# Kernel tuning notes

Measured on AMD Instinct MI355X. Metric: run time of the kernel, lower is better.

The kernel has to match this reference:

```python
import jax, jax.numpy as jnp
import numpy as np
from jax import lax


def setup_inputs() -> dict:
    key = jax.random.key(0)
    k1, k2, k3 = jax.random.split(key, 3)
    X = jax.random.normal(k1, (8192, 8192), dtype=jnp.float32)
    K = jax.random.normal(k2, (7, 7), dtype=jnp.float32)
    bias = jax.random.normal(k3, (1,), dtype=jnp.float32)
    return {"X": X, "K": K, "bias": bias}


def reference(X, K, bias):
    # Valid 2D cross-correlation of X [H, W] with K [kh, kw], plus scalar bias.
    # Output shape: [H - kh + 1, W - kw + 1].
    lhs = X[None, None, :, :]          # NCHW, N=C=1
    rhs = K[None, None, :, :]          # OIHW, O=I=1
    out = lax.conv_general_dilated(
        lhs, rhs,
        window_strides=(1, 1),
        padding='VALID',
        dimension_numbers=('NCHW', 'OIHW', 'NCHW'),
    )
    return out[0, 0] + bias[0]
```

## Files before the change

### kernel.cpp

```cpp
#include <hip/hip_runtime.h>
#include <hip/hip_bf16.h>

#define IN_N    8192
#define OUT_N   8186
#define KS      7

#define SCOLS   512
#define OCOLS   496
#define NSTRIP  17
#define NSEG    60
#define NBLK    (NSTRIP * NSEG)
#define NROWB   38
#define LSTR    1040
#define NT8     31
#define TOTSTEP 512

typedef __bf16 bf16x8 __attribute__((ext_vector_type(8)));
typedef float  f32x4  __attribute__((ext_vector_type(4)));

union BFU { __bf16 h; unsigned short u; };
__device__ __forceinline__ unsigned short f2bf(float f) {
    BFU c; c.h = (__bf16)f; return c.u;
}

template<bool G>
__device__ __forceinline__ void run_strip(
    const float* __restrict__ X, float* __restrict__ out,
    char* sb, const bf16x8* bfrag, float bv,
    int X0, int s0, int s1, int tid)
{
    const int lane = tid & 63;
    const int wv   = tid >> 6;
    const int lo   = lane & 15;
    const int hi   = lane >> 4;
    const int p    = tid >> 7;
    const int cg   = tid & 127;
    const int ccol = X0 + 4 * cg;
    const int wcol = cg * 8;

    int wbase = (16 * s0 + 22 + p) % NROWB;

    int roff[KS];
    #pragma unroll
    for (int ky = 0; ky < KS; ++ky)
        roff[ky] = ((16 * s0 + lo + ky) % NROWB) * LSTR + 16 * hi;

    #pragma unroll
    for (int k = 0; k < 11; ++k) {
        int r = 16 * s0 + 2 * k + p;
        int c = ccol;
        if (G) { r = min(r, IN_N - 1); c = min(c, IN_N - 4); }
        float4 v = *(const float4*)(X + (size_t)r * IN_N + c);
        ushort4 h;
        h.x = f2bf(v.x); h.y = f2bf(v.y); h.z = f2bf(v.z); h.w = f2bf(v.w);
        const int slot = (16 * s0 + 2 * k + p) % NROWB;
        *(ushort4*)(sb + slot * LSTR + wcol) = h;
    }
    asm volatile("s_waitcnt lgkmcnt(0)" ::: "memory");
    __builtin_amdgcn_s_barrier();
    __builtin_amdgcn_sched_barrier(0);

    float4 ld[8];
    for (int s = s0; s < s1; ++s) {
        const int Y = 16 * s;
        const bool pre = (s + 1 < s1);

        if (pre) {
            #pragma unroll
            for (int k = 0; k < 8; ++k) {
                int r = Y + 22 + 2 * k + p;
                int c = ccol;
                if (G) { r = min(r, IN_N - 1); c = min(c, IN_N - 4); }
                ld[k] = *(const float4*)(X + (size_t)r * IN_N + c);
            }
        }
        __builtin_amdgcn_sched_barrier(0);

        for (int t8 = wv; t8 < NT8; t8 += 4) {
            const int off = 32 * t8;
            f32x4 accA = { bv, bv, bv, bv };
            f32x4 accB = { 0.f, 0.f, 0.f, 0.f };
            bf16x8 a0 = *(const bf16x8*)(sb + roff[0] + off);
            bf16x8 a1 = *(const bf16x8*)(sb + roff[1] + off);
            bf16x8 a2 = *(const bf16x8*)(sb + roff[2] + off);
            bf16x8 a3 = *(const bf16x8*)(sb + roff[3] + off);
            bf16x8 a4 = *(const bf16x8*)(sb + roff[4] + off);
            bf16x8 a5 = *(const bf16x8*)(sb + roff[5] + off);
            bf16x8 a6 = *(const bf16x8*)(sb + roff[6] + off);
            accA = __builtin_amdgcn_mfma_f32_16x16x32_bf16(bfrag[0], a0, accA, 0, 0, 0);
            accB = __builtin_amdgcn_mfma_f32_16x16x32_bf16(bfrag[1], a1, accB, 0, 0, 0);
            accA = __builtin_amdgcn_mfma_f32_16x16x32_bf16(bfrag[2], a2, accA, 0, 0, 0);
            accB = __builtin_amdgcn_mfma_f32_16x16x32_bf16(bfrag[3], a3, accB, 0, 0, 0);
            accA = __builtin_amdgcn_mfma_f32_16x16x32_bf16(bfrag[4], a4, accA, 0, 0, 0);
            accB = __builtin_amdgcn_mfma_f32_16x16x32_bf16(bfrag[5], a5, accB, 0, 0, 0);
            accA = __builtin_amdgcn_mfma_f32_16x16x32_bf16(bfrag[6], a6, accA, 0, 0, 0);
            const f32x4 acc = accA + accB;

            const int oy = Y + lo;
            const int ox = X0 + 16 * t8 + 4 * hi;
            if constexpr (!G) {
                float2* po = (float2*)(out + (size_t)oy * OUT_N + ox);
                po[0] = make_float2(acc[0], acc[1]);
                po[1] = make_float2(acc[2], acc[3]);
            } else {
                if (oy < OUT_N) {
                    #pragma unroll
                    for (int r = 0; r < 4; ++r)
                        if (ox + r < OUT_N) out[(size_t)oy * OUT_N + ox + r] = acc[r];
                }
            }
        }
        __builtin_amdgcn_sched_barrier(0);

        if (pre) {
            #pragma unroll
            for (int k = 0; k < 8; ++k) {
                ushort4 h;
                h.x = f2bf(ld[k].x); h.y = f2bf(ld[k].y);
                h.z = f2bf(ld[k].z); h.w = f2bf(ld[k].w);
                int slot = wbase + 2 * k;
                if (slot >= NROWB) slot -= NROWB;
                *(ushort4*)(sb + slot * LSTR + wcol) = h;
            }
            asm volatile("s_waitcnt lgkmcnt(0)" ::: "memory");
            __builtin_amdgcn_s_barrier();
            __builtin_amdgcn_sched_barrier(0);
        }

        wbase += 16; if (wbase >= NROWB) wbase -= NROWB;
        #pragma unroll
        for (int ky = 0; ky < KS; ++ky) {
            roff[ky] += 16 * LSTR;
            if (roff[ky] >= NROWB * LSTR) roff[ky] -= NROWB * LSTR;
        }
    }
}

__global__ __launch_bounds__(256, 4)
void conv7x7_roll4(const float* __restrict__ X, const float* __restrict__ Kw,
                   const float* __restrict__ bias, float* __restrict__ out) {
    __shared__ __align__(16) char sb[NROWB * LSTR];

    const int tid  = threadIdx.x;
    const int lane = tid & 63;
    const int lo   = lane & 15;
    const int hi   = lane >> 4;

    const int orig = blockIdx.x;
    const int xcd  = orig & 7;
    const int idx  = orig >> 3;
    const int wg   = (xcd < 4 ? xcd * 128 : 4 * 128 + (xcd - 4) * 127) + idx;
    const int seg   = wg / NSTRIP;
    const int strip = wg - seg * NSTRIP;

    const int X0 = strip * OCOLS;
    const int s0 = (TOTSTEP * seg) / NSEG;
    const int s1 = (TOTSTEP * (seg + 1)) / NSEG;

    bf16x8 bfrag[KS];
    #pragma unroll
    for (int ky = 0; ky < KS; ++ky) {
        bf16x8 bv;
        #pragma unroll
        for (int e = 0; e < 8; ++e) {
            const int d = 8 * hi + e - lo;
            bv[e] = (__bf16)((d >= 0 && d < KS) ? Kw[ky * KS + d] : 0.0f);
        }
        bfrag[ky] = bv;
    }
    const float b = bias[0];

    if (strip < NSTRIP - 1 && seg < NSEG - 1)
        run_strip<false>(X, out, sb, bfrag, b, X0, s0, s1, tid);
    else
        run_strip<true >(X, out, sb, bfrag, b, X0, s0, s1, tid);
}

extern "C" void kernel_launch(void* const* d_in, const int* in_sizes, int n_in,
                              void* d_out, int out_size, void* d_ws, size_t ws_size,
                              hipStream_t stream) {
    const float* X    = (const float*)d_in[0];
    const float* Kw   = (const float*)d_in[1];
    const float* bias = (const float*)d_in[2];
    float* out = (float*)d_out;

    conv7x7_roll4<<<dim3(NBLK), dim3(256), 0, stream>>>(X, Kw, bias, out);
}
```

Before: 149.3 us.

## Stage MFMA outputs in LDS for row-contiguous stores and narrow the strips

MFMA results now go into an LDS output buffer, and after a barrier each wave writes whole output rows contiguously instead of scattering 16-byte fragments across 16 rows. The strip width shrinks from 512 to 320 columns and the grid grows to 27x28 blocks, with the load mapping and XCD remap reworked to match. The goal is more coalesced global stores. In exchange it adds a barrier per step, more LDS use, and more halo overhead from the narrower strips, and launch bounds drop to 2 blocks per CU.

```diff
diff --git a/kernel.cpp b/kernel.cpp
--- a/kernel.cpp
+++ b/kernel.cpp
@@ -5,18 +5,21 @@
 #define OUT_N   8186
 #define KS      7
 
-#define SCOLS   512
-#define OCOLS   496
-#define NSTRIP  17
-#define NSEG    60
+#define SCOLS   320
+#define OCOLS   304
+#define NSTRIP  27
+#define NSEG    28
 #define NBLK    (NSTRIP * NSEG)
 #define NROWB   38
-#define LSTR    1040
-#define NT8     31
+#define LSTR    656
+#define OSTR    1232
+#define NT8     19
+#define NLD     5
 #define TOTSTEP 512
 
 typedef __bf16 bf16x8 __attribute__((ext_vector_type(8)));
 typedef float  f32x4  __attribute__((ext_vector_type(4)));
+typedef float  f32x2  __attribute__((ext_vector_type(2)));
 
 union BFU { __bf16 h; unsigned short u; };
 __device__ __forceinline__ unsigned short f2bf(float f) {
@@ -26,50 +29,54 @@
 template<bool G>
 __device__ __forceinline__ void run_strip(
     const float* __restrict__ X, float* __restrict__ out,
-    char* sb, const bf16x8* bfrag, float bv,
+    char* ring, char* obuf, const bf16x8* bfrag, float bv,
     int X0, int s0, int s1, int tid)
 {
     const int lane = tid & 63;
     const int wv   = tid >> 6;
     const int lo   = lane & 15;
     const int hi   = lane >> 4;
-    const int p    = tid >> 7;
-    const int cg   = tid & 127;
-    const int ccol = X0 + 4 * cg;
-    const int wcol = cg * 8;
-
-    int wbase = (16 * s0 + 22 + p) % NROWB;
-
+
+    int srow16[NLD], scol16[NLD], wslot[NLD];
+    #pragma unroll
+    for (int k = 0; k < NLD; ++k) {
+        const int g = k * 256 + tid;
+        srow16[k] = g / 80;
+        scol16[k] = (g - srow16[k] * 80) * 4;
+        wslot[k]  = (16 * s0 + 22 + srow16[k]) % NROWB;
+    }
     int roff[KS];
     #pragma unroll
     for (int ky = 0; ky < KS; ++ky)
         roff[ky] = ((16 * s0 + lo + ky) % NROWB) * LSTR + 16 * hi;
 
     #pragma unroll
-    for (int k = 0; k < 11; ++k) {
-        int r = 16 * s0 + 2 * k + p;
-        int c = ccol;
-        if (G) { r = min(r, IN_N - 1); c = min(c, IN_N - 4); }
-        float4 v = *(const float4*)(X + (size_t)r * IN_N + c);
-        ushort4 h;
-        h.x = f2bf(v.x); h.y = f2bf(v.y); h.z = f2bf(v.z); h.w = f2bf(v.w);
-        const int slot = (16 * s0 + 2 * k + p) % NROWB;
-        *(ushort4*)(sb + slot * LSTR + wcol) = h;
+    for (int k = 0; k < 7; ++k) {
+        const int g = k * 256 + tid;
+        if (g < 1760) {
+            const int pr = g / 80;
+            const int pc = (g - pr * 80) * 4;
+            int r = 16 * s0 + pr, c = X0 + pc;
+            if (G) { r = min(r, IN_N - 1); c = min(c, IN_N - 4); }
+            float4 v = *(const float4*)(X + (size_t)r * IN_N + c);
+            ushort4 h;
+            h.x = f2bf(v.x); h.y = f2bf(v.y); h.z = f2bf(v.z); h.w = f2bf(v.w);
+            *(ushort4*)(ring + ((16 * s0 + pr) % NROWB) * LSTR + pc * 2) = h;
+        }
     }
     asm volatile("s_waitcnt lgkmcnt(0)" ::: "memory");
     __builtin_amdgcn_s_barrier();
     __builtin_amdgcn_sched_barrier(0);
 
-    float4 ld[8];
+    float4 ld[NLD];
     for (int s = s0; s < s1; ++s) {
         const int Y = 16 * s;
         const bool pre = (s + 1 < s1);
 
         if (pre) {
             #pragma unroll
-            for (int k = 0; k < 8; ++k) {
-                int r = Y + 22 + 2 * k + p;
-                int c = ccol;
+            for (int k = 0; k < NLD; ++k) {
+                int r = Y + 22 + srow16[k], c = X0 + scol16[k];
                 if (G) { r = min(r, IN_N - 1); c = min(c, IN_N - 4); }
                 ld[k] = *(const float4*)(X + (size_t)r * IN_N + c);
             }
@@ -80,13 +87,13 @@
             const int off = 32 * t8;
             f32x4 accA = { bv, bv, bv, bv };
             f32x4 accB = { 0.f, 0.f, 0.f, 0.f };
-            bf16x8 a0 = *(const bf16x8*)(sb + roff[0] + off);
-            bf16x8 a1 = *(const bf16x8*)(sb + roff[1] + off);
-            bf16x8 a2 = *(const bf16x8*)(sb + roff[2] + off);
-            bf16x8 a3 = *(const bf16x8*)(sb + roff[3] + off);
-            bf16x8 a4 = *(const bf16x8*)(sb + roff[4] + off);
-            bf16x8 a5 = *(const bf16x8*)(sb + roff[5] + off);
-            bf16x8 a6 = *(const bf16x8*)(sb + roff[6] + off);
+            bf16x8 a0 = *(const bf16x8*)(ring + roff[0] + off);
+            bf16x8 a1 = *(const bf16x8*)(ring + roff[1] + off);
+            bf16x8 a2 = *(const bf16x8*)(ring + roff[2] + off);
+            bf16x8 a3 = *(const bf16x8*)(ring + roff[3] + off);
+            bf16x8 a4 = *(const bf16x8*)(ring + roff[4] + off);
+            bf16x8 a5 = *(const bf16x8*)(ring + roff[5] + off);
+            bf16x8 a6 = *(const bf16x8*)(ring + roff[6] + off);
             accA = __builtin_amdgcn_mfma_f32_16x16x32_bf16(bfrag[0], a0, accA, 0, 0, 0);
             accB = __builtin_amdgcn_mfma_f32_16x16x32_bf16(bfrag[1], a1, accB, 0, 0, 0);
             accA = __builtin_amdgcn_mfma_f32_16x16x32_bf16(bfrag[2], a2, accA, 0, 0, 0);
@@ -95,18 +102,42 @@
             accB = __builtin_amdgcn_mfma_f32_16x16x32_bf16(bfrag[5], a5, accB, 0, 0, 0);
             accA = __builtin_amdgcn_mfma_f32_16x16x32_bf16(bfrag[6], a6, accA, 0, 0, 0);
             const f32x4 acc = accA + accB;
-
-            const int oy = Y + lo;
-            const int ox = X0 + 16 * t8 + 4 * hi;
+            *(f32x4*)(obuf + lo * OSTR + (16 * t8 + 4 * hi) * 4) = acc;
+        }
+        asm volatile("s_waitcnt lgkmcnt(0)" ::: "memory");
+        __builtin_amdgcn_s_barrier();
+        __builtin_amdgcn_sched_barrier(0);
+
+        #pragma unroll
+        for (int j = 0; j < 4; ++j) {
+            const int row = wv + 4 * j;
+            const int oy  = Y + row;
+            const size_t base = (size_t)oy * OUT_N + X0;
             if constexpr (!G) {
-                float2* po = (float2*)(out + (size_t)oy * OUT_N + ox);
-                po[0] = make_float2(acc[0], acc[1]);
-                po[1] = make_float2(acc[2], acc[3]);
+                {
+                    const int f = lane;
+                    f32x4 v = *(const f32x4*)(obuf + row * OSTR + f * 16);
+                    const f32x2 v0 = { v[0], v[1] }, v1 = { v[2], v[3] };
+                    *(f32x2*)(out + base + 4 * f)     = v0;
+                    *(f32x2*)(out + base + 4 * f + 2) = v1;
+                }
+                if (lane < 12) {
+                    const int f = lane + 64;
+                    f32x4 v = *(const f32x4*)(obuf + row * OSTR + f * 16);
+                    const f32x2 v0 = { v[0], v[1] }, v1 = { v[2], v[3] };
+                    *(f32x2*)(out + base + 4 * f)     = v0;
+                    *(f32x2*)(out + base + 4 * f + 2) = v1;
+                }
             } else {
                 if (oy < OUT_N) {
-                    #pragma unroll
-                    for (int r = 0; r < 4; ++r)
-                        if (ox + r < OUT_N) out[(size_t)oy * OUT_N + ox + r] = acc[r];
+                    for (int f = lane; f < 76; f += 64) {
+                        f32x4 v = *(const f32x4*)(obuf + row * OSTR + f * 16);
+                        #pragma unroll
+                        for (int e = 0; e < 4; ++e) {
+                            const int c = X0 + 4 * f + e;
+                            if (c < OUT_N) out[(size_t)oy * OUT_N + c] = v[e];
+                        }
+                    }
                 }
             }
         }
@@ -114,20 +145,21 @@
 
         if (pre) {
             #pragma unroll
-            for (int k = 0; k < 8; ++k) {
+            for (int k = 0; k < NLD; ++k) {
                 ushort4 h;
                 h.x = f2bf(ld[k].x); h.y = f2bf(ld[k].y);
                 h.z = f2bf(ld[k].z); h.w = f2bf(ld[k].w);
-                int slot = wbase + 2 * k;
-                if (slot >= NROWB) slot -= NROWB;
-                *(ushort4*)(sb + slot * LSTR + wcol) = h;
+                *(ushort4*)(ring + wslot[k] * LSTR + scol16[k] * 2) = h;
             }
             asm volatile("s_waitcnt lgkmcnt(0)" ::: "memory");
             __builtin_amdgcn_s_barrier();
             __builtin_amdgcn_sched_barrier(0);
         }
 
-        wbase += 16; if (wbase >= NROWB) wbase -= NROWB;
+        #pragma unroll
+        for (int k = 0; k < NLD; ++k) {
+            wslot[k] += 16; if (wslot[k] >= NROWB) wslot[k] -= NROWB;
+        }
         #pragma unroll
         for (int ky = 0; ky < KS; ++ky) {
             roff[ky] += 16 * LSTR;
@@ -136,10 +168,11 @@
     }
 }
 
-__global__ __launch_bounds__(256, 4)
-void conv7x7_roll4(const float* __restrict__ X, const float* __restrict__ Kw,
-                   const float* __restrict__ bias, float* __restrict__ out) {
-    __shared__ __align__(16) char sb[NROWB * LSTR];
+__global__ __launch_bounds__(256, 2)
+void conv7x7_gather(const float* __restrict__ X, const float* __restrict__ Kw,
+                    const float* __restrict__ bias, float* __restrict__ out) {
+    __shared__ __align__(16) char ring[NROWB * LSTR];
+    __shared__ __align__(16) char obuf[16 * OSTR];
 
     const int tid  = threadIdx.x;
     const int lane = tid & 63;
@@ -149,7 +182,7 @@
     const int orig = blockIdx.x;
     const int xcd  = orig & 7;
     const int idx  = orig >> 3;
-    const int wg   = (xcd < 4 ? xcd * 128 : 4 * 128 + (xcd - 4) * 127) + idx;
+    const int wg   = (xcd < 4 ? xcd * 95 : 4 * 95 + (xcd - 4) * 94) + idx;
     const int seg   = wg / NSTRIP;
     const int strip = wg - seg * NSTRIP;
 
@@ -171,9 +204,9 @@
     const float b = bias[0];
 
     if (strip < NSTRIP - 1 && seg < NSEG - 1)
-        run_strip<false>(X, out, sb, bfrag, b, X0, s0, s1, tid);
+        run_strip<false>(X, out, ring, obuf, bfrag, b, X0, s0, s1, tid);
     else
-        run_strip<true >(X, out, sb, bfrag, b, X0, s0, s1, tid);
+        run_strip<true >(X, out, ring, obuf, bfrag, b, X0, s0, s1, tid);
 }
 
 extern "C" void kernel_launch(void* const* d_in, const int* in_sizes, int n_in,
@@ -184,5 +217,5 @@
     const float* bias = (const float*)d_in[2];
     float* out = (float*)d_out;
 
-    conv7x7_roll4<<<dim3(NBLK), dim3(256), 0, stream>>>(X, Kw, bias, out);
-}
+    conv7x7_gather<<<dim3(NBLK), dim3(256), 0, stream>>>(X, Kw, bias, out);
+}
```

Result: slower. 159.0 us (+6.5%).
